# Kernel tuning notes

Measured on AMD Instinct MI355X. Metric: run time of the kernel, lower is better.

The kernel has to match this reference:

```python
import jax, jax.numpy as jnp
import numpy as np

_LOG2PI = 0.9189385332046727
_NUM_VARS = 256   # D
_NUM_UNITS = 64   # K
_BATCH = 2048     # B
_NUM_LEVELS = 8   # log2(D)


def setup_inputs() -> dict:
    key = jax.random.key(0)
    D, K, B = _NUM_VARS, _NUM_UNITS, _BATCH
    inp = {}
    inp["x"] = jax.random.normal(jax.random.fold_in(key, 0), (B, 1, D), dtype=jnp.float32)
    inp["mu"] = jax.random.normal(jax.random.fold_in(key, 1), (D, K), dtype=jnp.float32)
    inp["log_sigma"] = 0.1 * jax.random.normal(jax.random.fold_in(key, 2), (D, K), dtype=jnp.float32)
    # input-layer bookkeeping: each fold reads one (permuted) variable of x
    inp["in_scope_idx"] = jax.random.permutation(jax.random.fold_in(key, 3), D)[:, None]
    F = D
    for l in range(1, _NUM_LEVELS + 1):
        # fold bookkeeping: irregular pairing of previous-layer folds (permutation -> valid partition)
        inp[f"fold_idx{l}"] = jax.random.permutation(jax.random.fold_in(key, 10 + l), F).reshape(F // 2, 2)
        F //= 2
        inp[f"w{l}"] = jax.random.normal(jax.random.fold_in(key, 100 + l), (F, K, K), dtype=jnp.float32)
    return inp


def _circuit(x, mu, log_sigma, ws, in_scope_idx, fold_idxs):
    # input layer gather: x (B,C,D) -> x[..., idx] (B,C,F,s) -> permute (F,C,B,s)
    xg = jnp.transpose(x[..., in_scope_idx], (2, 1, 0, 3))  # (D,1,B,1)
    xv = xg[:, 0, :, 0]  # (D,B): C=1, scope size 1
    # Gaussian input layer, log densities: (F=D, B, K)
    z = (xv[:, :, None] - mu[:, None, :]) * jnp.exp(-log_sigma)[:, None, :]
    out = -0.5 * z * z - log_sigma[:, None, :] - _LOG2PI
    for fidx, w in zip(fold_idxs, ws):
        # folded Hadamard product layer: gather (F,2,B,K) via bookkeeping, add in log-space
        h = out[fidx].sum(axis=1)  # (F,B,K)
        # folded dense sum layer: y[f,b,j] = logsumexp_k( log softmax(w)[f,j,k] + h[f,b,k] )
        wp = jax.nn.softmax(w, axis=-1)  # (F,K,K)
        m = jnp.max(h, axis=-1, keepdims=True)
        out = jnp.log(jnp.einsum('fbk,fjk->fbj', jnp.exp(h - m), wp)) + m  # (F,B,K)
    # final bookkeeping: (F_out=1, B, K) -> transpose(0,1) -> (B, 1, K)
    return jnp.transpose(out, (1, 0, 2))


def reference(x, mu, log_sigma, w1, w2, w3, w4, w5, w6, w7, w8,
              in_scope_idx, fold_idx1, fold_idx2, fold_idx3, fold_idx4,
              fold_idx5, fold_idx6, fold_idx7, fold_idx8):
    ws = (w1, w2, w3, w4, w5, w6, w7, w8)
    fold_idxs = (fold_idx1, fold_idx2, fold_idx3, fold_idx4,
                 fold_idx5, fold_idx6, fold_idx7, fold_idx8)
    return _circuit(x, mu, log_sigma, ws, in_scope_idx, fold_idxs)
```

## Files before the change

### kernel.cpp

```cpp
#include <hip/hip_runtime.h>
#include <math.h>

#define LOG2PI_F  0.9189385332046727f
#define INV_LN2_F 1.4426950408889634f
#define LN2_F     0.6931471805599453f
#define SROW      72

typedef short bf16x8 __attribute__((ext_vector_type(8)));
typedef float f32x4  __attribute__((ext_vector_type(4)));

struct __align__(16) Op { int w; int c0; int c1; int pad; };

#define WS_WBJ   0u
#define WS_A     2097152u
#define WS_B     2162688u
#define WS_C     2228224u
#define WS_XT    2293760u
#define WS_SCHED 4390912u
#define WS_L4A   4395008u
#define WS_L4M   8589312u

__device__ __forceinline__ short bfr(float f) {
    unsigned int u = __float_as_uint(f);
    u += 0x7fffu + ((u >> 16) & 1u);
    return (short)(u >> 16);
}

struct F8v { float v[8]; };
__device__ __forceinline__ F8v ld8(const float* p) {
    F8v r;
    float4 a = *(const float4*)p;
    float4 b = *(const float4*)(p + 4);
    r.v[0]=a.x; r.v[1]=a.y; r.v[2]=a.z; r.v[3]=a.w;
    r.v[4]=b.x; r.v[5]=b.y; r.v[6]=b.z; r.v[7]=b.w;
    return r;
}

__device__ __forceinline__ void up8(int4 v, float* o) {
    o[0] = __uint_as_float(((unsigned)v.x) << 16);
    o[1] = __uint_as_float(((unsigned)v.x) & 0xffff0000u);
    o[2] = __uint_as_float(((unsigned)v.y) << 16);
    o[3] = __uint_as_float(((unsigned)v.y) & 0xffff0000u);
    o[4] = __uint_as_float(((unsigned)v.z) << 16);
    o[5] = __uint_as_float(((unsigned)v.z) & 0xffff0000u);
    o[6] = __uint_as_float(((unsigned)v.w) << 16);
    o[7] = __uint_as_float(((unsigned)v.w) & 0xffff0000u);
}

__device__ __forceinline__ float rmax16(const float hv[16]) {
    float m01 = fmaxf(hv[0], hv[1]),  m23 = fmaxf(hv[2], hv[3]);
    float m45 = fmaxf(hv[4], hv[5]),  m67 = fmaxf(hv[6], hv[7]);
    float m89 = fmaxf(hv[8], hv[9]),  mab = fmaxf(hv[10], hv[11]);
    float mcd = fmaxf(hv[12], hv[13]), mef = fmaxf(hv[14], hv[15]);
    float hm = fmaxf(fmaxf(fmaxf(m01, m23), fmaxf(m45, m67)),
                     fmaxf(fmaxf(m89, mab), fmaxf(mcd, mef)));
    hm = fmaxf(hm, __shfl_xor(hm, 16, 64));
    hm = fmaxf(hm, __shfl_xor(hm, 32, 64));
    return hm;
}

__device__ __forceinline__ void pack_p(const float e[16], bf16x8& a0, bf16x8& a1) {
    int4 p0, p1;
    p0.x = __builtin_amdgcn_perm(__float_as_uint(e[1]),  __float_as_uint(e[0]),  0x07060302u);
    p0.y = __builtin_amdgcn_perm(__float_as_uint(e[3]),  __float_as_uint(e[2]),  0x07060302u);
    p0.z = __builtin_amdgcn_perm(__float_as_uint(e[5]),  __float_as_uint(e[4]),  0x07060302u);
    p0.w = __builtin_amdgcn_perm(__float_as_uint(e[7]),  __float_as_uint(e[6]),  0x07060302u);
    p1.x = __builtin_amdgcn_perm(__float_as_uint(e[9]),  __float_as_uint(e[8]),  0x07060302u);
    p1.y = __builtin_amdgcn_perm(__float_as_uint(e[11]), __float_as_uint(e[10]), 0x07060302u);
    p1.z = __builtin_amdgcn_perm(__float_as_uint(e[13]), __float_as_uint(e[12]), 0x07060302u);
    p1.w = __builtin_amdgcn_perm(__float_as_uint(e[15]), __float_as_uint(e[14]), 0x07060302u);
    a0 = *(bf16x8*)&p0;
    a1 = *(bf16x8*)&p1;
}

__global__ __launch_bounds__(256) void prep_kernel(
    const float* __restrict__ w1, const float* __restrict__ w2,
    const float* __restrict__ w3, const float* __restrict__ w4,
    const float* __restrict__ w5, const float* __restrict__ w6,
    const float* __restrict__ w7, const float* __restrict__ w8,
    const float* __restrict__ mu, const float* __restrict__ ls,
    const float* __restrict__ x,  const int* __restrict__ scope,
    const int* __restrict__ f1, const int* __restrict__ f2,
    const int* __restrict__ f3, const int* __restrict__ f4,
    const int* __restrict__ f5, const int* __restrict__ f6,
    const int* __restrict__ f7, const int* __restrict__ f8,
    char* __restrict__ ws)
{
    const int bx = blockIdx.x, t = threadIdx.x;
    if (bx < 255) {
        __shared__ float smax[64], ssum[64];
        const int g = bx;
        const float* src;
        if (g < 128)      src = w1 + g * 4096;
        else if (g < 192) src = w2 + (g - 128) * 4096;
        else if (g < 224) src = w3 + (g - 192) * 4096;
        else if (g < 240) src = w4 + (g - 224) * 4096;
        else if (g < 248) src = w5 + (g - 240) * 4096;
        else if (g < 252) src = w6 + (g - 248) * 4096;
        else              src = (g < 254) ? (w7 + (g - 252) * 4096) : w8;
        const int lane = t & 63, wv = t >> 6;
        for (int r = 0; r < 16; ++r) {
            int j = wv * 16 + r;
            float v = src[j * 64 + lane];
            float mx = v;
            for (int d = 1; d < 64; d <<= 1) mx = fmaxf(mx, __shfl_xor(mx, d, 64));
            float e = __expf(v - mx);
            float sm = e;
            for (int d = 1; d < 64; d <<= 1) sm += __shfl_xor(sm, d, 64);
            if (lane == 0) { smax[j] = mx; ssum[j] = sm; }
        }
        __syncthreads();
        unsigned short* dst = (unsigned short*)(ws + WS_WBJ) + g * 4096;
        for (int u = 0; u < 16; ++u) {
            int idx = u * 256 + t;
            int j = idx >> 6, k = idx & 63;
            float v = __expf(src[idx] - smax[j]) / ssum[j];
            int f  = ((j >> 4) << 1) | (k >> 5);
            int ln = (((k >> 3) & 3) << 4) | (j & 15);
            dst[(f * 64 + ln) * 8 + (k & 7)] = (unsigned short)bfr(v);
        }
    } else if (bx < 319) {
        const int idx = (bx - 255) * 256 + t;
        float m = mu[idx], l = ls[idx];
        float is2 = __expf(-2.0f * l);
        ((float*)(ws + WS_A))[idx] = -0.5f * is2 * INV_LN2_F;
        ((float*)(ws + WS_B))[idx] = m * is2 * INV_LN2_F;
        ((float*)(ws + WS_C))[idx] = (-0.5f * m * m * is2 - l - LOG2PI_F) * INV_LN2_F;
    } else if (bx < 575) {
        const int bb = bx - 319;
        const int sd = scope[t];
        float* xT = (float*)(ws + WS_XT);
        #pragma unroll
        for (int i = 0; i < 8; ++i) {
            int b = bb * 8 + i;
            xT[t * 2048 + b] = x[b * 256 + sd];
        }
    } else {
        __shared__ int sf[512];
        for (int i = t; i < 256; i += 256) sf[i]        = f1[i];
        for (int i = t; i < 128; i += 256) sf[256 + i]  = f2[i];
        for (int i = t; i <  64; i += 256) sf[384 + i]  = f3[i];
        for (int i = t; i <  32; i += 256) sf[448 + i]  = f4[i];
        for (int i = t; i <  16; i += 256) sf[480 + i]  = f5[i];
        for (int i = t; i <   8; i += 256) sf[496 + i]  = f6[i];
        for (int i = t; i <   4; i += 256) sf[504 + i]  = f7[i];
        for (int i = t; i <   2; i += 256) sf[508 + i]  = f8[i];
        __syncthreads();
        const int* F1 = &sf[0];   const int* F2 = &sf[256];
        const int* F3 = &sf[384]; const int* F4 = &sf[448];
        const int* F5 = &sf[480]; const int* F6 = &sf[496];
        const int* F7 = &sf[504]; const int* F8 = &sf[508];
        Op* base = (Op*)(ws + WS_SCHED);
        if (t < 16) {
            Op* o = base + t * 15;
            int r0 = F4[2*t], r1 = F4[2*t+1];
            int P[4] = { F3[2*r0], F3[2*r0+1], F3[2*r1], F3[2*r1+1] };
            #pragma unroll
            for (int j = 0; j < 4; ++j) {
                int L0 = F2[2*P[j]], L1 = F2[2*P[j]+1];
                o[2*j]   = { L0 * 4096, F1[2*L0], F1[2*L0+1], 0 };
                o[2*j+1] = { L1 * 4096, F1[2*L1], F1[2*L1+1], 0 };
                o[8+j]   = { (128 + P[j]) * 4096, 0, 0, 0 };
            }
            o[12] = { (192 + r0) * 4096, 0, 0, 0 };
            o[13] = { (192 + r1) * 4096, 0, 0, 0 };
            o[14] = { (224 + t)  * 4096, 0, 0, 0 };
        } else if (t == 16) {
            Op* o = base + 240;
            int g[4] = { F7[2*F8[0]], F7[2*F8[0]+1], F7[2*F8[1]], F7[2*F8[1]+1] };
            #pragma unroll
            for (int a = 0; a < 4; ++a) {
                int l0 = F6[2*g[a]], l1 = F6[2*g[a]+1];
                o[2*a]   = { (240 + l0) * 4096, F5[2*l0], F5[2*l0+1], 0 };
                o[2*a+1] = { (240 + l1) * 4096, F5[2*l1], F5[2*l1+1], 0 };
                o[8+a]   = { (248 + g[a]) * 4096, 0, 0, 0 };
            }
            o[12] = { (252 + F8[0]) * 4096, 0, 0, 0 };
            o[13] = { (252 + F8[1]) * 4096, 0, 0, 0 };
            o[14] = { 254 * 4096, 0, 0, 0 };
        }
    }
}

__device__ __forceinline__ void load_bfrag(const unsigned short* __restrict__ wbJ,
                                           int w, int lane, int4 bf[8]) {
    const int4* wp = (const int4*)(wbJ + w);
    #pragma unroll
    for (int f = 0; f < 8; ++f) bf[f] = wp[f * 64 + lane];
}

__device__ __forceinline__ void prod_norm(const float av[16], const float bv[16],
                                          float MA, float MB,
                                          float p[16], float& Mrow) {
    float pv[16];
    #pragma unroll
    for (int i = 0; i < 16; ++i) pv[i] = av[i] * bv[i];
    const float rm = rmax16(pv);
    const int e = (int)((__float_as_uint(rm) >> 23) & 0xFF) - 127;
    #pragma unroll
    for (int i = 0; i < 16; ++i) p[i] = ldexpf(pv[i], -e);
    Mrow = MA + MB + (float)e;
}

__device__ __forceinline__ void gauss_p(const Op& op,
    const float* __restrict__ xT, const float* __restrict__ Ag,
    const float* __restrict__ Bg, const float* __restrict__ Cg,
    int b0, int m, int q, float p[16], float& Mrow)
{
    const int d0 = op.c0, d1 = op.c1;
    const float xv0 = xT[d0 * 2048 + b0 + m];
    const float xv1 = xT[d1 * 2048 + b0 + m];
    const float x0s = xv0 * xv0, x1s = xv1 * xv1;
    float hv[16];
    #pragma unroll
    for (int kh = 0; kh < 2; ++kh) {
        const int kb = kh * 32 + q * 8;
        F8v A0 = ld8(Ag + d0*64 + kb), B0 = ld8(Bg + d0*64 + kb);
        F8v C0 = ld8(Cg + d0*64 + kb);
        F8v A1 = ld8(Ag + d1*64 + kb), B1 = ld8(Bg + d1*64 + kb);
        F8v C1 = ld8(Cg + d1*64 + kb);
        #pragma unroll
        for (int i = 0; i < 8; ++i) {
            float t0 = fmaf(A0.v[i], x0s, C0.v[i]);
            t0 = fmaf(B0.v[i], xv0, t0);
            float t1 = fmaf(A1.v[i], x1s, C1.v[i]);
            t1 = fmaf(B1.v[i], xv1, t1);
            hv[kh*8+i] = t0 + t1;
        }
    }
    const float hm = rmax16(hv);
    #pragma unroll
    for (int i = 0; i < 16; ++i) p[i] = __builtin_amdgcn_exp2f(hv[i] - hm);
    Mrow = hm;
}

__device__ __forceinline__ void gprod_p(const Op& op,
    const unsigned short* __restrict__ inAcc, const float* __restrict__ inM,
    int b0, int m, int q, float p[16], float& Mrow)
{
    const int4* A4 = (const int4*)(inAcc + (size_t)(op.c0 * 2048 + b0 + m) * 64);
    const int4* B4 = (const int4*)(inAcc + (size_t)(op.c1 * 2048 + b0 + m) * 64);
    float av[16], bv[16];
    up8(A4[q], av); up8(A4[4+q], av + 8);
    up8(B4[q], bv); up8(B4[4+q], bv + 8);
    prod_norm(av, bv, inM[op.c0 * 2048 + b0 + m], inM[op.c1 * 2048 + b0 + m], p, Mrow);
}

__device__ __forceinline__ void slot_prod(const unsigned short* slotS, const float* Mslot,
                                          int sA, int sB, int m, int q,
                                          float p[16], float& Mrow)
{
    const int4* A4 = (const int4*)(slotS + sA * 16 * SROW + m * SROW);
    const int4* B4 = (const int4*)(slotS + sB * 16 * SROW + m * SROW);
    float av[16], bv[16];
    up8(A4[q], av); up8(A4[4+q], av + 8);
    up8(B4[q], bv); up8(B4[4+q], bv + 8);
    prod_norm(av, bv, Mslot[sA * 16 + m], Mslot[sB * 16 + m], p, Mrow);
}

__device__ __forceinline__ void mfma8(const float p[16], const int4 bf[8], f32x4 acc[4]) {
    bf16x8 a0, a1;
    pack_p(p, a0, a1);
    #pragma unroll
    for (int jt = 0; jt < 4; ++jt) {
        f32x4 z = {0.f, 0.f, 0.f, 0.f};
        z = __builtin_amdgcn_mfma_f32_16x16x32_bf16(a0, *(bf16x8*)&bf[jt*2+0], z, 0, 0, 0);
        z = __builtin_amdgcn_mfma_f32_16x16x32_bf16(a1, *(bf16x8*)&bf[jt*2+1], z, 0, 0, 0);
        acc[jt] = z;
    }
}

__device__ __forceinline__ void store_slot(unsigned short* slotS, float* Mslot,
                                           int sl, const f32x4 acc[4], float Mrow,
                                           int m, int q)
{
    unsigned short* S = slotS + sl * 16 * SROW;
    #pragma unroll
    for (int jt = 0; jt < 4; ++jt)
        #pragma unroll
        for (int r = 0; r < 4; ++r)
            S[(q*4 + r) * SROW + jt*16 + m] = (unsigned short)bfr(acc[jt][r]);
    if (q == 0) Mslot[sl * 16 + m] = Mrow;
}

__device__ __forceinline__ void wave_fence() {
    __builtin_amdgcn_wave_barrier();
    __builtin_amdgcn_s_waitcnt(0xC07F);
    __builtin_amdgcn_wave_barrier();
}

template<int MODE>
__global__ __launch_bounds__(128, 4) void circuit_coop(
    const unsigned short* __restrict__ wbJ,
    const Op* __restrict__ schedG, int nsub,
    const float* __restrict__ xT, const float* __restrict__ Ag,
    const float* __restrict__ Bg, const float* __restrict__ Cg,
    const unsigned short* __restrict__ inAcc, const float* __restrict__ inM,
    unsigned short* __restrict__ outAcc, float* __restrict__ outM,
    float* __restrict__ outLog)
{
    __shared__ __align__(16) unsigned short slotS[8 * 16 * SROW];
    __shared__ float Mslot[8 * 16];
    __shared__ Op ops[16];

    const int t    = threadIdx.x;
    const int wv   = t >> 6;
    const int lane = t & 63;
    const int m    = lane & 15;
    const int q    = lane >> 4;
    const int s    = blockIdx.x % nsub;
    const int b0   = (blockIdx.x / nsub) * 16;

    if (t < 15) *(int4*)&ops[t] = ((const int4*)(schedG + s * 15))[t];
    __syncthreads();

    #pragma unroll
    for (int pr = 0; pr < 2; ++pr) {
        const int slA = 4 * wv + 2 * pr;
        const int slB = slA + 1;
        const Op opA = ops[slA], opB = ops[slB];
        int4 bfA[8], bfB[8];
        load_bfrag(wbJ, opA.w, lane, bfA);
        load_bfrag(wbJ, opB.w, lane, bfB);
        float pA[16], pB[16], MA, MB;
        if (MODE == 0) {
            gauss_p(opA, xT, Ag, Bg, Cg, b0, m, q, pA, MA);
            gauss_p(opB, xT, Ag, Bg, Cg, b0, m, q, pB, MB);
        } else {
            gprod_p(opA, inAcc, inM, b0, m, q, pA, MA);
            gprod_p(opB, inAcc, inM, b0, m, q, pB, MB);
        }
        f32x4 accA[4], accB[4];
        mfma8(pA, bfA, accA);
        mfma8(pB, bfB, accB);
        store_slot(slotS, Mslot, slA, accA, MA, m, q);
        store_slot(slotS, Mslot, slB, accB, MB, m, q);
    }
    wave_fence();

    {
        const int jA = 2 * wv, jB = 2 * wv + 1;
        const Op opA = ops[8 + jA], opB = ops[8 + jB];
        int4 bfA[8], bfB[8];
        load_bfrag(wbJ, opA.w, lane, bfA);
        load_bfrag(wbJ, opB.w, lane, bfB);
        float pA[16], pB[16], MA, MB;
        slot_prod(slotS, Mslot, 2*jA, 2*jA + 1, m, q, pA, MA);
        slot_prod(slotS, Mslot, 2*jB, 2*jB + 1, m, q, pB, MB);
        f32x4 accA[4], accB[4];
        mfma8(pA, bfA, accA);
        mfma8(pB, bfB, accB);
        store_slot(slotS, Mslot, 2*jA, accA, MA, m, q);
        store_slot(slotS, Mslot, 2*jB, accB, MB, m, q);
    }
    wave_fence();

    {
        const Op op = ops[12 + wv];
        int4 bf[8];
        load_bfrag(wbJ, op.w, lane, bf);
        float p[16], Mrow;
        slot_prod(slotS, Mslot, 4*wv, 4*wv + 2, m, q, p, Mrow);
        f32x4 acc[4];
        mfma8(p, bf, acc);
        store_slot(slotS, Mslot, 4*wv, acc, Mrow, m, q);
    }
    __syncthreads();

    if (wv == 0) {
        const Op op = ops[14];
        int4 bf[8];
        load_bfrag(wbJ, op.w, lane, bf);
        float p[16], Mrow;
        slot_prod(slotS, Mslot, 0, 4, m, q, p, Mrow);
        f32x4 acc[4];
        mfma8(p, bf, acc);
        if (MODE == 0) {
            const int rowOff = s * 2048;
            #pragma unroll
            for (int jt = 0; jt < 4; ++jt)
                #pragma unroll
                for (int r = 0; r < 4; ++r)
                    outAcc[(size_t)(rowOff + b0 + q*4 + r) * 64 + jt*16 + m] =
                        (unsigned short)bfr(acc[jt][r]);
            if (q == 0) outM[rowOff + b0 + m] = Mrow;
        } else {
            float mr[4];
            #pragma unroll
            for (int r = 0; r < 4; ++r) mr[r] = __shfl(Mrow, q * 4 + r, 64);
            #pragma unroll
            for (int jt = 0; jt < 4; ++jt)
                #pragma unroll
                for (int r = 0; r < 4; ++r)
                    outLog[(b0 + q*4 + r) * 64 + jt*16 + m] =
                        (__builtin_amdgcn_logf(acc[jt][r]) + mr[r]) * LN2_F;
        }
    }
}

extern "C" void kernel_launch(void* const* d_in, const int* in_sizes, int n_in,
                              void* d_out, int out_size, void* d_ws, size_t ws_size,
                              hipStream_t stream) {
    const float* x     = (const float*)d_in[0];
    const float* mu    = (const float*)d_in[1];
    const float* lsg   = (const float*)d_in[2];
    const int*   scope = (const int*)d_in[3];
    const int*   f1 = (const int*)d_in[4];   const float* w1 = (const float*)d_in[5];
    const int*   f2 = (const int*)d_in[6];   const float* w2 = (const float*)d_in[7];
    const int*   f3 = (const int*)d_in[8];   const float* w3 = (const float*)d_in[9];
    const int*   f4 = (const int*)d_in[10];  const float* w4 = (const float*)d_in[11];
    const int*   f5 = (const int*)d_in[12];  const float* w5 = (const float*)d_in[13];
    const int*   f6 = (const int*)d_in[14];  const float* w6 = (const float*)d_in[15];
    const int*   f7 = (const int*)d_in[16];  const float* w7 = (const float*)d_in[17];
    const int*   f8 = (const int*)d_in[18];  const float* w8 = (const float*)d_in[19];

    char* ws = (char*)d_ws;
    const unsigned short* wbJ = (const unsigned short*)(ws + WS_WBJ);
    const float* Ag  = (const float*)(ws + WS_A);
    const float* Bg  = (const float*)(ws + WS_B);
    const float* Cg  = (const float*)(ws + WS_C);
    const float* xT  = (const float*)(ws + WS_XT);
    const Op*    sch = (const Op*)(ws + WS_SCHED);
    unsigned short* L4A = (unsigned short*)(ws + WS_L4A);
    float*          L4M = (float*)(ws + WS_L4M);

    prep_kernel<<<576, 256, 0, stream>>>(w1, w2, w3, w4, w5, w6, w7, w8,
                                         mu, lsg, x, scope,
                                         f1, f2, f3, f4, f5, f6, f7, f8, ws);

    circuit_coop<0><<<2048, 128, 0, stream>>>(
        wbJ, sch, 16,
        xT, Ag, Bg, Cg,
        nullptr, nullptr,
        L4A, L4M, nullptr);

    circuit_coop<1><<<128, 128, 0, stream>>>(
        wbJ, sch + 240, 1,
        nullptr, nullptr, nullptr, nullptr,
        L4A, L4M,
        nullptr, nullptr, (float*)d_out);
}
```

Measured before the change: 145.7 us.

## Widen circuit blocks to 32 batch rows and four waves, reusing weight fragments

```diff
diff --git a/kernel.cpp b/kernel.cpp
--- a/kernel.cpp
+++ b/kernel.cpp
@@ -205,11 +205,11 @@
 __device__ __forceinline__ void gauss_p(const Op& op,
     const float* __restrict__ xT, const float* __restrict__ Ag,
     const float* __restrict__ Bg, const float* __restrict__ Cg,
-    int b0, int m, int q, float p[16], float& Mrow)
+    int rowStart, int m, int q, float p[16], float& Mrow)
 {
     const int d0 = op.c0, d1 = op.c1;
-    const float xv0 = xT[d0 * 2048 + b0 + m];
-    const float xv1 = xT[d1 * 2048 + b0 + m];
+    const float xv0 = xT[d0 * 2048 + rowStart + m];
+    const float xv1 = xT[d1 * 2048 + rowStart + m];
     const float x0s = xv0 * xv0, x1s = xv1 * xv1;
     float hv[16];
     #pragma unroll
@@ -236,26 +236,26 @@
 
 __device__ __forceinline__ void gprod_p(const Op& op,
     const unsigned short* __restrict__ inAcc, const float* __restrict__ inM,
-    int b0, int m, int q, float p[16], float& Mrow)
-{
-    const int4* A4 = (const int4*)(inAcc + (size_t)(op.c0 * 2048 + b0 + m) * 64);
-    const int4* B4 = (const int4*)(inAcc + (size_t)(op.c1 * 2048 + b0 + m) * 64);
+    int rowStart, int m, int q, float p[16], float& Mrow)
+{
+    const int4* A4 = (const int4*)(inAcc + (size_t)(op.c0 * 2048 + rowStart + m) * 64);
+    const int4* B4 = (const int4*)(inAcc + (size_t)(op.c1 * 2048 + rowStart + m) * 64);
     float av[16], bv[16];
     up8(A4[q], av); up8(A4[4+q], av + 8);
     up8(B4[q], bv); up8(B4[4+q], bv + 8);
-    prod_norm(av, bv, inM[op.c0 * 2048 + b0 + m], inM[op.c1 * 2048 + b0 + m], p, Mrow);
+    prod_norm(av, bv, inM[op.c0 * 2048 + rowStart + m], inM[op.c1 * 2048 + rowStart + m], p, Mrow);
 }
 
 __device__ __forceinline__ void slot_prod(const unsigned short* slotS, const float* Mslot,
-                                          int sA, int sB, int m, int q,
+                                          int sA, int sB, int rowBase, int m, int q,
                                           float p[16], float& Mrow)
 {
-    const int4* A4 = (const int4*)(slotS + sA * 16 * SROW + m * SROW);
-    const int4* B4 = (const int4*)(slotS + sB * 16 * SROW + m * SROW);
+    const int4* A4 = (const int4*)(slotS + sA * 32 * SROW + (rowBase + m) * SROW);
+    const int4* B4 = (const int4*)(slotS + sB * 32 * SROW + (rowBase + m) * SROW);
     float av[16], bv[16];
     up8(A4[q], av); up8(A4[4+q], av + 8);
     up8(B4[q], bv); up8(B4[4+q], bv + 8);
-    prod_norm(av, bv, Mslot[sA * 16 + m], Mslot[sB * 16 + m], p, Mrow);
+    prod_norm(av, bv, Mslot[sA * 32 + rowBase + m], Mslot[sB * 32 + rowBase + m], p, Mrow);
 }
 
 __device__ __forceinline__ void mfma8(const float p[16], const int4 bf[8], f32x4 acc[4]) {
@@ -271,16 +271,16 @@
 }
 
 __device__ __forceinline__ void store_slot(unsigned short* slotS, float* Mslot,
-                                           int sl, const f32x4 acc[4], float Mrow,
-                                           int m, int q)
-{
-    unsigned short* S = slotS + sl * 16 * SROW;
+                                           int sl, int rowBase, const f32x4 acc[4],
+                                           float Mrow, int m, int q)
+{
+    unsigned short* S = slotS + sl * 32 * SROW;
     #pragma unroll
     for (int jt = 0; jt < 4; ++jt)
         #pragma unroll
         for (int r = 0; r < 4; ++r)
-            S[(q*4 + r) * SROW + jt*16 + m] = (unsigned short)bfr(acc[jt][r]);
-    if (q == 0) Mslot[sl * 16 + m] = Mrow;
+            S[(rowBase + q*4 + r) * SROW + jt*16 + m] = (unsigned short)bfr(acc[jt][r]);
+    if (q == 0) Mslot[sl * 32 + rowBase + m] = Mrow;
 }
 
 __device__ __forceinline__ void wave_fence() {
@@ -290,17 +290,17 @@
 }
 
 template<int MODE>
-__global__ __launch_bounds__(128, 4) void circuit_coop(
+__global__ __launch_bounds__(256, 4) void circuit_coop(
     const unsigned short* __restrict__ wbJ,
-    const Op* __restrict__ schedG, int nsub,
+    const Op* __restrict__ schedG, int ntile,
     const float* __restrict__ xT, const float* __restrict__ Ag,
     const float* __restrict__ Bg, const float* __restrict__ Cg,
     const unsigned short* __restrict__ inAcc, const float* __restrict__ inM,
     unsigned short* __restrict__ outAcc, float* __restrict__ outM,
     float* __restrict__ outLog)
 {
-    __shared__ __align__(16) unsigned short slotS[8 * 16 * SROW];
-    __shared__ float Mslot[8 * 16];
+    __shared__ __align__(16) unsigned short slotS[8 * 32 * SROW];
+    __shared__ float Mslot[8 * 32];
     __shared__ Op ops[16];
 
     const int t    = threadIdx.x;
@@ -308,62 +308,62 @@
     const int lane = t & 63;
     const int m    = lane & 15;
     const int q    = lane >> 4;
-    const int s    = blockIdx.x % nsub;
-    const int b0   = (blockIdx.x / nsub) * 16;
+    const int s    = blockIdx.x / ntile;
+    const int b0   = (blockIdx.x % ntile) * 32;
 
     if (t < 15) *(int4*)&ops[t] = ((const int4*)(schedG + s * 15))[t];
     __syncthreads();
 
     #pragma unroll
-    for (int pr = 0; pr < 2; ++pr) {
-        const int slA = 4 * wv + 2 * pr;
-        const int slB = slA + 1;
-        const Op opA = ops[slA], opB = ops[slB];
-        int4 bfA[8], bfB[8];
-        load_bfrag(wbJ, opA.w, lane, bfA);
-        load_bfrag(wbJ, opB.w, lane, bfB);
-        float pA[16], pB[16], MA, MB;
-        if (MODE == 0) {
-            gauss_p(opA, xT, Ag, Bg, Cg, b0, m, q, pA, MA);
-            gauss_p(opB, xT, Ag, Bg, Cg, b0, m, q, pB, MB);
-        } else {
-            gprod_p(opA, inAcc, inM, b0, m, q, pA, MA);
-            gprod_p(opB, inAcc, inM, b0, m, q, pB, MB);
-        }
-        f32x4 accA[4], accB[4];
-        mfma8(pA, bfA, accA);
-        mfma8(pB, bfB, accB);
-        store_slot(slotS, Mslot, slA, accA, MA, m, q);
-        store_slot(slotS, Mslot, slB, accB, MB, m, q);
-    }
-    wave_fence();
-
-    {
-        const int jA = 2 * wv, jB = 2 * wv + 1;
-        const Op opA = ops[8 + jA], opB = ops[8 + jB];
-        int4 bfA[8], bfB[8];
-        load_bfrag(wbJ, opA.w, lane, bfA);
-        load_bfrag(wbJ, opB.w, lane, bfB);
-        float pA[16], pB[16], MA, MB;
-        slot_prod(slotS, Mslot, 2*jA, 2*jA + 1, m, q, pA, MA);
-        slot_prod(slotS, Mslot, 2*jB, 2*jB + 1, m, q, pB, MB);
-        f32x4 accA[4], accB[4];
-        mfma8(pA, bfA, accA);
-        mfma8(pB, bfB, accB);
-        store_slot(slotS, Mslot, 2*jA, accA, MA, m, q);
-        store_slot(slotS, Mslot, 2*jB, accB, MB, m, q);
-    }
-    wave_fence();
-
-    {
-        const Op op = ops[12 + wv];
+    for (int i = 0; i < 2; ++i) {
+        const int sl = 2 * wv + i;
+        const Op op = ops[sl];
         int4 bf[8];
         load_bfrag(wbJ, op.w, lane, bf);
-        float p[16], Mrow;
-        slot_prod(slotS, Mslot, 4*wv, 4*wv + 2, m, q, p, Mrow);
-        f32x4 acc[4];
-        mfma8(p, bf, acc);
-        store_slot(slotS, Mslot, 4*wv, acc, Mrow, m, q);
+        float p0[16], p1[16], M0, M1;
+        if (MODE == 0) {
+            gauss_p(op, xT, Ag, Bg, Cg, b0,      m, q, p0, M0);
+            gauss_p(op, xT, Ag, Bg, Cg, b0 + 16, m, q, p1, M1);
+        } else {
+            gprod_p(op, inAcc, inM, b0,      m, q, p0, M0);
+            gprod_p(op, inAcc, inM, b0 + 16, m, q, p1, M1);
+        }
+        f32x4 acc0[4], acc1[4];
+        mfma8(p0, bf, acc0);
+        mfma8(p1, bf, acc1);
+        store_slot(slotS, Mslot, sl, 0,  acc0, M0, m, q);
+        store_slot(slotS, Mslot, sl, 16, acc1, M1, m, q);
+    }
+    wave_fence();
+
+    {
+        const Op op = ops[8 + wv];
+        int4 bf[8];
+        load_bfrag(wbJ, op.w, lane, bf);
+        float p0[16], p1[16], M0, M1;
+        slot_prod(slotS, Mslot, 2*wv, 2*wv + 1, 0,  m, q, p0, M0);
+        slot_prod(slotS, Mslot, 2*wv, 2*wv + 1, 16, m, q, p1, M1);
+        f32x4 acc0[4], acc1[4];
+        mfma8(p0, bf, acc0);
+        mfma8(p1, bf, acc1);
+        store_slot(slotS, Mslot, 2*wv, 0,  acc0, M0, m, q);
+        store_slot(slotS, Mslot, 2*wv, 16, acc1, M1, m, q);
+    }
+    __syncthreads();
+
+    if ((wv & 1) == 0) {
+        const int u = wv >> 1;
+        const Op op = ops[12 + u];
+        int4 bf[8];
+        load_bfrag(wbJ, op.w, lane, bf);
+        float p0[16], p1[16], M0, M1;
+        slot_prod(slotS, Mslot, 4*u, 4*u + 2, 0,  m, q, p0, M0);
+        slot_prod(slotS, Mslot, 4*u, 4*u + 2, 16, m, q, p1, M1);
+        f32x4 acc0[4], acc1[4];
+        mfma8(p0, bf, acc0);
+        mfma8(p1, bf, acc1);
+        store_slot(slotS, Mslot, 4*u, 0,  acc0, M0, m, q);
+        store_slot(slotS, Mslot, 4*u, 16, acc1, M1, m, q);
     }
     __syncthreads();
 
@@ -371,29 +371,43 @@
         const Op op = ops[14];
         int4 bf[8];
         load_bfrag(wbJ, op.w, lane, bf);
-        float p[16], Mrow;
-        slot_prod(slotS, Mslot, 0, 4, m, q, p, Mrow);
-        f32x4 acc[4];
-        mfma8(p, bf, acc);
+        float p0[16], p1[16], M0, M1;
+        slot_prod(slotS, Mslot, 0, 4, 0,  m, q, p0, M0);
+        slot_prod(slotS, Mslot, 0, 4, 16, m, q, p1, M1);
+        f32x4 acc0[4], acc1[4];
+        mfma8(p0, bf, acc0);
+        mfma8(p1, bf, acc1);
         if (MODE == 0) {
-            const int rowOff = s * 2048;
+            const int rowOff = s * 2048 + b0;
             #pragma unroll
             for (int jt = 0; jt < 4; ++jt)
                 #pragma unroll
-                for (int r = 0; r < 4; ++r)
-                    outAcc[(size_t)(rowOff + b0 + q*4 + r) * 64 + jt*16 + m] =
-                        (unsigned short)bfr(acc[jt][r]);
-            if (q == 0) outM[rowOff + b0 + m] = Mrow;
+                for (int r = 0; r < 4; ++r) {
+                    outAcc[(size_t)(rowOff +      q*4 + r) * 64 + jt*16 + m] =
+                        (unsigned short)bfr(acc0[jt][r]);
+                    outAcc[(size_t)(rowOff + 16 + q*4 + r) * 64 + jt*16 + m] =
+                        (unsigned short)bfr(acc1[jt][r]);
+                }
+            if (q == 0) {
+                outM[rowOff + m]      = M0;
+                outM[rowOff + 16 + m] = M1;
+            }
         } else {
-            float mr[4];
+            float mr0[4], mr1[4];
             #pragma unroll
-            for (int r = 0; r < 4; ++r) mr[r] = __shfl(Mrow, q * 4 + r, 64);
+            for (int r = 0; r < 4; ++r) {
+                mr0[r] = __shfl(M0, q * 4 + r, 64);
+                mr1[r] = __shfl(M1, q * 4 + r, 64);
+            }
             #pragma unroll
             for (int jt = 0; jt < 4; ++jt)
                 #pragma unroll
-                for (int r = 0; r < 4; ++r)
-                    outLog[(b0 + q*4 + r) * 64 + jt*16 + m] =
-                        (__builtin_amdgcn_logf(acc[jt][r]) + mr[r]) * LN2_F;
+                for (int r = 0; r < 4; ++r) {
+                    outLog[(b0 +      q*4 + r) * 64 + jt*16 + m] =
+                        (__builtin_amdgcn_logf(acc0[jt][r]) + mr0[r]) * LN2_F;
+                    outLog[(b0 + 16 + q*4 + r) * 64 + jt*16 + m] =
+                        (__builtin_amdgcn_logf(acc1[jt][r]) + mr1[r]) * LN2_F;
+                }
         }
     }
 }
@@ -428,14 +442,14 @@
                                          mu, lsg, x, scope,
                                          f1, f2, f3, f4, f5, f6, f7, f8, ws);
 
-    circuit_coop<0><<<2048, 128, 0, stream>>>(
-        wbJ, sch, 16,
+    circuit_coop<0><<<1024, 256, 0, stream>>>(
+        wbJ, sch, 64,
         xT, Ag, Bg, Cg,
         nullptr, nullptr,
         L4A, L4M, nullptr);
 
-    circuit_coop<1><<<128, 128, 0, stream>>>(
-        wbJ, sch + 240, 1,
+    circuit_coop<1><<<64, 256, 0, stream>>>(
+        wbJ, sch + 240, 64,
         nullptr, nullptr, nullptr, nullptr,
         L4A, L4M,
         nullptr, nullptr, (float*)d_out);
```

Result: faster. 139.5 us (-4.3%).
